# Performance work log

Hardware: AMD Instinct MI355X
Metric: run time of the kernel (lower is better)

## Reference

```python
import jax, jax.numpy as jnp
import numpy as np

S, B, T = 512, 256, 128


def setup_inputs() -> dict:
    key = jax.random.key(0)
    k1, k2, k3, k4, k5, k6 = jax.random.split(key, 6)
    emissions = jax.random.normal(k1, (S, B, T), dtype=jnp.float32)
    # realistic monotone mask: each sequence has a random length in [1, S]
    lengths = jax.random.randint(k2, (B,), 1, S + 1)
    mask = (jnp.arange(S)[:, None] < lengths[None, :]).astype(jnp.float32)  # [S,B]
    tags = jax.random.randint(k3, (S, B), 0, T)
    transitions = jax.random.normal(k4, (T, T), dtype=jnp.float32)
    start_transitions = jax.random.normal(k5, (T,), dtype=jnp.float32)
    stop_transitions = jax.random.normal(k6, (T,), dtype=jnp.float32)
    return {
        "emissions": emissions,
        "mask": mask,
        "tags": tags,
        "transitions": transitions,
        "start_transitions": start_transitions,
        "stop_transitions": stop_transitions,
    }


def reference(emissions, mask, tags, transitions, start_transitions, stop_transitions):
    seq_len, batch, num_tags = emissions.shape

    # ---- log-partition (forward algorithm) + viterbi score, fused scan ----
    init = start_transitions + emissions[0]  # [B,T]

    def part_step(carry, xs):
        fv, vv = carry  # forward var, viterbi var: [B,T]
        em, m = xs      # em: [B,T], m: [B]
        # scores[b, j, k] = em[b, j] + transitions[j, k]  (j=next tag, k=prev tag)
        scores = em[:, :, None] + transitions[None, :, :]          # [B,T,T]
        lse = jax.nn.logsumexp(fv[:, None, :] + scores, axis=2)     # [B,T]
        vmax = jnp.max(vv[:, None, :] + scores, axis=2)             # [B,T]
        fv = m[:, None] * lse + (1.0 - m)[:, None] * fv
        vv = m[:, None] * vmax + (1.0 - m)[:, None] * vv
        return (fv, vv), None

    (fv, vv), _ = jax.lax.scan(part_step, (init, init), (emissions[1:], mask[1:]))
    total_score = jax.nn.logsumexp(fv + stop_transitions, axis=1)   # [B]
    best_path_score = jnp.max(vv + stop_transitions, axis=1)        # [B]

    # ---- gold path score ----
    barange = jnp.arange(batch)
    tag0 = tags[0]
    rps0 = start_transitions[tag0] + emissions[0, barange, tag0] * mask[0]

    def rp_step(carry, xs):
        rps, prev = carry
        cur, em, m = xs  # cur:[B] int, em:[B,T], m:[B]
        rps = rps + transitions[prev, cur] * m
        rps = rps + jnp.take_along_axis(em, cur[:, None], axis=1)[:, 0] * m
        prev = jnp.where(m == 1.0, cur, prev)
        return (rps, prev), None

    (rps, prev), _ = jax.lax.scan(rp_step, (rps0, tag0), (tags[1:], emissions[1:], mask[1:]))
    real_path_score = rps + stop_transitions[prev]

    loss = jnp.mean(total_score - real_path_score)
    return loss, real_path_score, total_score, best_path_score
```

## Files before the change

### kernel.cpp

```cpp
#include <hip/hip_runtime.h>
#include <math.h>

#define S_LEN 512
#define BATCH 256
#define NTAG  128
#define EMSTRIDE (BATCH * NTAG)

typedef float f32x4 __attribute__((ext_vector_type(4)));

__device__ __forceinline__ int swz(int k) { return k + ((k >> 5) << 3); }

#define DPP_XOR1(x) __int_as_float(__builtin_amdgcn_mov_dpp(__float_as_int(x), 0xB1, 0xF, 0xF, false))
#define DPP_XOR2(x) __int_as_float(__builtin_amdgcn_mov_dpp(__float_as_int(x), 0x4E, 0xF, 0xF, false))

#define BAR() do {                                       \
    asm volatile("s_waitcnt lgkmcnt(0)" ::: "memory");   \
    __builtin_amdgcn_s_barrier();                        \
    __builtin_amdgcn_sched_barrier(0);                   \
  } while (0)

__device__ __forceinline__ float max3f(float a, float b, float c) {
  return fmaxf(fmaxf(a, b), c);
}

__global__ __launch_bounds__(512, 1)
void crf_fat_kernel(const float* __restrict__ emis,
                    const float* __restrict__ mask,
                    const int* __restrict__ tags,
                    const float* __restrict__ trans,
                    const float* __restrict__ startt,
                    const float* __restrict__ stopt,
                    float* __restrict__ out)
{
  const int blk = blockIdx.x;
  const int tid = threadIdx.x;

  __shared__ __align__(16) float sbuf[2][160];
  __shared__ float red[16];

  if (blk >= 2 * BATCH) {
    const int b = blk - 2 * BATCH;
    const int s = tid;
    float m  = mask[(size_t)s * BATCH + b];
    int  cur = tags[(size_t)s * BATCH + b];
    float part, lenp = m;
    if (s == 0) {
      part = startt[cur] + emis[(size_t)b * NTAG + cur] * m;
    } else {
      int prev = tags[(size_t)(s - 1) * BATCH + b];
      part = m * (trans[(size_t)prev * NTAG + cur] +
                  emis[((size_t)s * BATCH + b) * NTAG + cur]);
    }
#pragma unroll
    for (int d = 1; d <= 32; d <<= 1) {
      part += __shfl_xor(part, d);
      lenp += __shfl_xor(lenp, d);
    }
    const int glane = tid & 63, gwid = tid >> 6;
    if (glane == 0) { red[gwid] = part; red[8 + gwid] = lenp; }
    __syncthreads();
    if (tid == 0) {
      float rps = 0.f, lf = 0.f;
#pragma unroll
      for (int w = 0; w < 8; ++w) { rps += red[w]; lf += red[8 + w]; }
      int len = (int)(lf + 0.5f);
      int pf  = tags[(size_t)(len - 1) * BATCH + b];
      out[1 + b] = rps + stopt[pf];
    }
    return;
  }

  const int b    = blk >> 1;
  const int role = blk & 1;
  const int h    = tid & 3;
  const int j    = tid >> 2;
  const int lane = tid & 63;
  const int wid  = tid >> 6;
  const int base = 10 * h;

  int len;
  {
    float mv = mask[(size_t)tid * BATCH + b];
#pragma unroll
    for (int d = 1; d <= 32; d <<= 1) mv += __shfl_xor(mv, d);
    if (lane == 0) red[wid] = mv;
    __syncthreads();
    float ls = 0.f;
#pragma unroll
    for (int w = 0; w < 8; ++w) ls += red[w];
    len = (int)(ls + 0.5f);
    len = __builtin_amdgcn_readfirstlane(len);
  }

  const float* eb = emis + (size_t)b * NTAG + j;

  if (role == 0) {
    f32x4 E[8];
    {
      const float* tr = trans + (size_t)j * NTAG + 32 * h;
#pragma unroll
      for (int c = 0; c < 8; ++c) {
        f32x4 t = *(const f32x4*)(tr + 4 * c);
        E[c][0] = __expf(t[0]); E[c][1] = __expf(t[1]);
        E[c][2] = __expf(t[2]); E[c][3] = __expf(t[3]);
      }
    }
    if (h == 0) sbuf[0][swz(j)] = __expf(startt[j] + eb[0]);

    float e0 = eb[(size_t)1 * EMSTRIDE];
    float e1 = eb[(size_t)2 * EMSTRIDE];
    float e2 = eb[(size_t)3 * EMSTRIDE];
    float e3 = eb[(size_t)4 * EMSTRIDE];

    int Ew = 0, fin = 0;
    __syncthreads();

#define FSTEP(U, EMV, RENORM)                                                \
  {                                                                          \
    if (g + (U) >= len) { fin = (U) & 1; goto epi_f; }                       \
    const f32x4* wr = (const f32x4*)sbuf[(U) & 1];                           \
    float s0 = 0.f, s1 = 0.f, s2 = 0.f, s3 = 0.f, rw = 0.f;                  \
    _Pragma("unroll")                                                        \
    for (int c = 0; c < 8; ++c) {                                            \
      f32x4 w = wr[base + c];                                                \
      s0 = __builtin_fmaf(E[c][0], w[0], s0);                                \
      s1 = __builtin_fmaf(E[c][1], w[1], s1);                                \
      s2 = __builtin_fmaf(E[c][2], w[2], s2);                                \
      s3 = __builtin_fmaf(E[c][3], w[3], s3);                                \
      if (RENORM) { rw = max3f(rw, w[0], w[1]); rw = max3f(rw, w[2], w[3]); }\
    }                                                                        \
    float ex  = __expf(EMV);                                                 \
    float sum = (s0 + s1) + (s2 + s3);                                       \
    sum += DPP_XOR1(sum); sum += DPP_XOR2(sum);                              \
    float uf;                                                                \
    if (RENORM) {                                                            \
      rw = fmaxf(rw, DPP_XOR1(rw)); rw = fmaxf(rw, DPP_XOR2(rw));            \
      int ew = (int)((__float_as_uint(rw) >> 23) & 0xFF) - 126;              \
      Ew += ew;                                                              \
      float sw = __uint_as_float((unsigned)(127 - ew) << 23);                \
      uf = ex * sum * sw;                                                    \
    } else {                                                                 \
      uf = ex * sum;                                                         \
    }                                                                        \
    if (h == 0) sbuf[((U) + 1) & 1][swz(j)] = uf;                            \
    BAR();                                                                   \
  }

    for (int g = 1; g < S_LEN; g += 4) {
      int c0 = g + 4, c1 = g + 5, c2 = g + 6, c3 = g + 7;
      c0 = c0 < S_LEN ? c0 : S_LEN - 1;
      c1 = c1 < S_LEN ? c1 : S_LEN - 1;
      c2 = c2 < S_LEN ? c2 : S_LEN - 1;
      c3 = c3 < S_LEN ? c3 : S_LEN - 1;
      float n0 = eb[(size_t)c0 * EMSTRIDE];
      float n1 = eb[(size_t)c1 * EMSTRIDE];
      float n2 = eb[(size_t)c2 * EMSTRIDE];
      float n3 = eb[(size_t)c3 * EMSTRIDE];

      FSTEP(0, e0, 0)
      FSTEP(1, e1, 0)
      FSTEP(2, e2, 0)
      FSTEP(3, e3, 1)

      e0 = n0; e1 = n1; e2 = n2; e3 = n3;
    }
    fin = 0;

epi_f:
    {
      float W  = sbuf[fin][swz(j)];
      float es = __expf(stopt[j]);
      int q2 = fin ^ 1;
      if (h == 0) sbuf[q2][swz(j)] = W * es;
      __syncthreads();
      if (tid < 64) {
        float sA = sbuf[q2][swz(tid)] + sbuf[q2][swz(tid + 64)];
#pragma unroll
        for (int d = 1; d <= 32; d <<= 1) sA += __shfl_xor(sA, d);
        if (tid == 0) {
          const double LN2 = 0.6931471805599453;
          out[1 + BATCH + b] = (float)((double)Ew * LN2 + (double)__logf(sA));
        }
      }
    }
  } else {
    f32x4 T[8];
    {
      const float* tr = trans + (size_t)j * NTAG + 32 * h;
#pragma unroll
      for (int c = 0; c < 8; ++c) T[c] = *(const f32x4*)(tr + 4 * c);
    }
    if (h == 0) sbuf[0][swz(j)] = startt[j] + eb[0];

    float e0 = eb[(size_t)1 * EMSTRIDE];
    float e1 = eb[(size_t)2 * EMSTRIDE];
    float e2 = eb[(size_t)3 * EMSTRIDE];
    float e3 = eb[(size_t)4 * EMSTRIDE];

    int fin = 0;
    __syncthreads();

#define VSTEP(U, EMV)                                                        \
  {                                                                          \
    if (g + (U) >= len) { fin = (U) & 1; goto epi_v; }                       \
    const f32x4* vr = (const f32x4*)sbuf[(U) & 1];                           \
    float vmA = -3.0e38f, vmB = -3.0e38f;                                    \
    _Pragma("unroll")                                                        \
    for (int c = 0; c < 8; ++c) {                                            \
      f32x4 v = vr[base + c];                                                \
      vmA = max3f(vmA, v[0] + T[c][0], v[1] + T[c][1]);                      \
      vmB = max3f(vmB, v[2] + T[c][2], v[3] + T[c][3]);                      \
    }                                                                        \
    float vm = fmaxf(vmA, vmB);                                              \
    vm = fmaxf(vm, DPP_XOR1(vm)); vm = fmaxf(vm, DPP_XOR2(vm));              \
    float uv = EMV + vm;                                                     \
    if (h == 0) sbuf[((U) + 1) & 1][swz(j)] = uv;                            \
    BAR();                                                                   \
  }

    for (int g = 1; g < S_LEN; g += 4) {
      int c0 = g + 4, c1 = g + 5, c2 = g + 6, c3 = g + 7;
      c0 = c0 < S_LEN ? c0 : S_LEN - 1;
      c1 = c1 < S_LEN ? c1 : S_LEN - 1;
      c2 = c2 < S_LEN ? c2 : S_LEN - 1;
      c3 = c3 < S_LEN ? c3 : S_LEN - 1;
      float n0 = eb[(size_t)c0 * EMSTRIDE];
      float n1 = eb[(size_t)c1 * EMSTRIDE];
      float n2 = eb[(size_t)c2 * EMSTRIDE];
      float n3 = eb[(size_t)c3 * EMSTRIDE];

      VSTEP(0, e0)
      VSTEP(1, e1)
      VSTEP(2, e2)
      VSTEP(3, e3)

      e0 = n0; e1 = n1; e2 = n2; e3 = n3;
    }
    fin = 0;

epi_v:
    {
      float V = sbuf[fin][swz(j)];
      float a = V + stopt[j];
      int q2 = fin ^ 1;
      if (h == 0) sbuf[q2][swz(j)] = a;
      __syncthreads();
      if (tid < 64) {
        float mB = fmaxf(sbuf[q2][swz(tid)], sbuf[q2][swz(tid + 64)]);
#pragma unroll
        for (int d = 1; d <= 32; d <<= 1) mB = fmaxf(mB, __shfl_xor(mB, d));
        if (tid == 0) out[1 + 2 * BATCH + b] = mB;
      }
    }
  }
}

__global__ __launch_bounds__(256, 1)
void crf_loss_kernel(float* __restrict__ out)
{
  const int tid = threadIdx.x;
  float dft = out[1 + BATCH + tid] - out[1 + tid];
#pragma unroll
  for (int d = 1; d <= 32; d <<= 1) dft += __shfl_xor(dft, d);
  __shared__ float rs[4];
  const int lane = tid & 63, wid = tid >> 6;
  if (lane == 0) rs[wid] = dft;
  __syncthreads();
  if (tid == 0)
    out[0] = ((rs[0] + rs[1]) + (rs[2] + rs[3])) * (1.0f / BATCH);
}

extern "C" void kernel_launch(void* const* d_in, const int* in_sizes, int n_in,
                              void* d_out, int out_size, void* d_ws, size_t ws_size,
                              hipStream_t stream)
{
  const float* emis   = (const float*)d_in[0];
  const float* mask   = (const float*)d_in[1];
  const int*   tags   = (const int*)d_in[2];
  const float* trans  = (const float*)d_in[3];
  const float* startt = (const float*)d_in[4];
  const float* stopt  = (const float*)d_in[5];
  float* out = (float*)d_out;

  crf_fat_kernel<<<3 * BATCH, 512, 0, stream>>>(emis, mask, tags, trans,
                                                startt, stopt, out);
  crf_loss_kernel<<<1, 256, 0, stream>>>(out);
}
```

Baseline: 209.2 us.

## Split CRF recursions into forward and backward halves meeting at the midpoint

Splits each sequence's forward-algorithm and Viterbi recursions into a forward half and a backward half that run in separate blocks. The halves meet at the midpoint and are combined by a new kernel: a dot product for the log-partition and a max of sums for Viterbi. This roughly halves the serial chain of barrier-separated steps per block. It also shrinks blocks to 256 threads with 2 lanes per tag and packed 2-wide math, and adds workspace traffic plus an extra kernel launch.

```diff
diff --git a/kernel.cpp b/kernel.cpp
--- a/kernel.cpp
+++ b/kernel.cpp
@@ -7,11 +7,16 @@
 #define EMSTRIDE (BATCH * NTAG)
 
 typedef float f32x4 __attribute__((ext_vector_type(4)));
-
-__device__ __forceinline__ int swz(int k) { return k + ((k >> 5) << 3); }
+typedef float f32x2 __attribute__((ext_vector_type(2)));
+
+__device__ __forceinline__ int lidx(int k) { return k + ((k >> 6) << 2); }
+__device__ __forceinline__ f32x2 lo2(f32x4 v){ f32x2 r; r[0]=v[0]; r[1]=v[1]; return r; }
+__device__ __forceinline__ f32x2 hi2(f32x4 v){ f32x2 r; r[0]=v[2]; r[1]=v[3]; return r; }
+__device__ __forceinline__ f32x2 pmax2(f32x2 a, f32x2 b){
+  f32x2 r; r[0]=fmaxf(a[0],b[0]); r[1]=fmaxf(a[1],b[1]); return r;
+}
 
 #define DPP_XOR1(x) __int_as_float(__builtin_amdgcn_mov_dpp(__float_as_int(x), 0xB1, 0xF, 0xF, false))
-#define DPP_XOR2(x) __int_as_float(__builtin_amdgcn_mov_dpp(__float_as_int(x), 0x4E, 0xF, 0xF, false))
 
 #define BAR() do {                                       \
     asm volatile("s_waitcnt lgkmcnt(0)" ::: "memory");   \
@@ -19,50 +24,53 @@
     __builtin_amdgcn_sched_barrier(0);                   \
   } while (0)
 
-__device__ __forceinline__ float max3f(float a, float b, float c) {
-  return fmaxf(fmaxf(a, b), c);
-}
-
-__global__ __launch_bounds__(512, 1)
+__global__ __launch_bounds__(256, 1)
 void crf_fat_kernel(const float* __restrict__ emis,
                     const float* __restrict__ mask,
                     const int* __restrict__ tags,
                     const float* __restrict__ trans,
                     const float* __restrict__ startt,
                     const float* __restrict__ stopt,
+                    float* __restrict__ ws,
+                    int* __restrict__ ewbuf,
                     float* __restrict__ out)
 {
-  const int blk = blockIdx.x;
-  const int tid = threadIdx.x;
-
-  __shared__ __align__(16) float sbuf[2][160];
-  __shared__ float red[16];
-
-  if (blk >= 2 * BATCH) {
-    const int b = blk - 2 * BATCH;
-    const int s = tid;
-    float m  = mask[(size_t)s * BATCH + b];
-    int  cur = tags[(size_t)s * BATCH + b];
-    float part, lenp = m;
-    if (s == 0) {
-      part = startt[cur] + emis[(size_t)b * NTAG + cur] * m;
-    } else {
-      int prev = tags[(size_t)(s - 1) * BATCH + b];
-      part = m * (trans[(size_t)prev * NTAG + cur] +
-                  emis[((size_t)s * BATCH + b) * NTAG + cur]);
+  const int blk  = blockIdx.x;
+  const int tid  = threadIdx.x;
+  const int role = blk >> 8;
+  const int b    = blk & 255;
+  const int lane = tid & 63;
+  const int wid  = tid >> 6;
+
+  __shared__ __align__(16) float sbuf[2][144];
+  __shared__ float red[8];
+
+  if (role == 4) {
+    float part = 0.f, lenp = 0.f;
+#pragma unroll
+    for (int rep = 0; rep < 2; ++rep) {
+      int s = tid + rep * 256;
+      float m  = mask[(size_t)s * BATCH + b];
+      int  cur = tags[(size_t)s * BATCH + b];
+      if (s == 0) {
+        part += startt[cur] + emis[(size_t)b * NTAG + cur] * m;
+      } else {
+        int prev = tags[(size_t)(s - 1) * BATCH + b];
+        part += m * (trans[(size_t)prev * NTAG + cur] +
+                     emis[((size_t)s * BATCH + b) * NTAG + cur]);
+      }
+      lenp += m;
     }
 #pragma unroll
     for (int d = 1; d <= 32; d <<= 1) {
       part += __shfl_xor(part, d);
       lenp += __shfl_xor(lenp, d);
     }
-    const int glane = tid & 63, gwid = tid >> 6;
-    if (glane == 0) { red[gwid] = part; red[8 + gwid] = lenp; }
+    if (lane == 0) { red[wid] = part; red[4 + wid] = lenp; }
     __syncthreads();
     if (tid == 0) {
-      float rps = 0.f, lf = 0.f;
-#pragma unroll
-      for (int w = 0; w < 8; ++w) { rps += red[w]; lf += red[8 + w]; }
+      float rps = (red[0] + red[1]) + (red[2] + red[3]);
+      float lf  = (red[4] + red[5]) + (red[6] + red[7]);
       int len = (int)(lf + 0.5f);
       int pf  = tags[(size_t)(len - 1) * BATCH + b];
       out[1 + b] = rps + stopt[pf];
@@ -70,188 +78,332 @@
     return;
   }
 
-  const int b    = blk >> 1;
-  const int role = blk & 1;
-  const int h    = tid & 3;
-  const int j    = tid >> 2;
-  const int lane = tid & 63;
-  const int wid  = tid >> 6;
-  const int base = 10 * h;
+  const int p    = tid >> 1;
+  const int h    = tid & 1;
+  const int widx = lidx(p);
 
   int len;
   {
-    float mv = mask[(size_t)tid * BATCH + b];
+    float mv = mask[(size_t)tid * BATCH + b] +
+               mask[(size_t)(tid + 256) * BATCH + b];
 #pragma unroll
     for (int d = 1; d <= 32; d <<= 1) mv += __shfl_xor(mv, d);
     if (lane == 0) red[wid] = mv;
     __syncthreads();
-    float ls = 0.f;
-#pragma unroll
-    for (int w = 0; w < 8; ++w) ls += red[w];
+    float ls = (red[0] + red[1]) + (red[2] + red[3]);
     len = (int)(ls + 0.5f);
     len = __builtin_amdgcn_readfirstlane(len);
   }
-
-  const float* eb = emis + (size_t)b * NTAG + j;
+  const int sm     = (len - 1) >> 1;
+  const int nsteps = len - 1 - sm;
+  const float* eb  = emis + (size_t)b * NTAG + p;
 
   if (role == 0) {
-    f32x4 E[8];
-    {
-      const float* tr = trans + (size_t)j * NTAG + 32 * h;
-#pragma unroll
-      for (int c = 0; c < 8; ++c) {
+    f32x2 E2[32];
+    {
+      const float* tr = trans + (size_t)p * NTAG + 64 * h;
+#pragma unroll
+      for (int c = 0; c < 16; ++c) {
         f32x4 t = *(const f32x4*)(tr + 4 * c);
-        E[c][0] = __expf(t[0]); E[c][1] = __expf(t[1]);
-        E[c][2] = __expf(t[2]); E[c][3] = __expf(t[3]);
+        f32x2 a, bb;
+        a[0] = __expf(t[0]); a[1] = __expf(t[1]);
+        bb[0] = __expf(t[2]); bb[1] = __expf(t[3]);
+        E2[2*c] = a; E2[2*c+1] = bb;
       }
     }
-    if (h == 0) sbuf[0][swz(j)] = __expf(startt[j] + eb[0]);
-
+    if (h == 0) sbuf[0][widx] = __expf(startt[p] + eb[0]);
     float e0 = eb[(size_t)1 * EMSTRIDE];
     float e1 = eb[(size_t)2 * EMSTRIDE];
     float e2 = eb[(size_t)3 * EMSTRIDE];
     float e3 = eb[(size_t)4 * EMSTRIDE];
-
     int Ew = 0, fin = 0;
     __syncthreads();
 
-#define FSTEP(U, EMV, RENORM)                                                \
-  {                                                                          \
-    if (g + (U) >= len) { fin = (U) & 1; goto epi_f; }                       \
-    const f32x4* wr = (const f32x4*)sbuf[(U) & 1];                           \
-    float s0 = 0.f, s1 = 0.f, s2 = 0.f, s3 = 0.f, rw = 0.f;                  \
-    _Pragma("unroll")                                                        \
-    for (int c = 0; c < 8; ++c) {                                            \
-      f32x4 w = wr[base + c];                                                \
-      s0 = __builtin_fmaf(E[c][0], w[0], s0);                                \
-      s1 = __builtin_fmaf(E[c][1], w[1], s1);                                \
-      s2 = __builtin_fmaf(E[c][2], w[2], s2);                                \
-      s3 = __builtin_fmaf(E[c][3], w[3], s3);                                \
-      if (RENORM) { rw = max3f(rw, w[0], w[1]); rw = max3f(rw, w[2], w[3]); }\
-    }                                                                        \
-    float ex  = __expf(EMV);                                                 \
-    float sum = (s0 + s1) + (s2 + s3);                                       \
-    sum += DPP_XOR1(sum); sum += DPP_XOR2(sum);                              \
-    float uf;                                                                \
-    if (RENORM) {                                                            \
-      rw = fmaxf(rw, DPP_XOR1(rw)); rw = fmaxf(rw, DPP_XOR2(rw));            \
-      int ew = (int)((__float_as_uint(rw) >> 23) & 0xFF) - 126;              \
-      Ew += ew;                                                              \
-      float sw = __uint_as_float((unsigned)(127 - ew) << 23);                \
-      uf = ex * sum * sw;                                                    \
-    } else {                                                                 \
-      uf = ex * sum;                                                         \
-    }                                                                        \
-    if (h == 0) sbuf[((U) + 1) & 1][swz(j)] = uf;                            \
-    BAR();                                                                   \
+#define FSTEP(U, EXV, RENORM)                                                 \
+  {                                                                           \
+    if (g + (U) > sm) { fin = (U) & 1; goto epi_f; }                          \
+    const f32x4* wr = (const f32x4*)(sbuf[(U) & 1] + 68 * h);                 \
+    f32x2 a0 = {0.f, 0.f}, a1 = {0.f, 0.f}, r2 = {0.f, 0.f};                  \
+    _Pragma("unroll")                                                         \
+    for (int c = 0; c < 16; ++c) {                                            \
+      f32x4 w = wr[c];                                                        \
+      f32x2 wl = lo2(w), wh = hi2(w);                                         \
+      a0 = a0 + E2[2*c] * wl;                                                 \
+      a1 = a1 + E2[2*c+1] * wh;                                               \
+      if (RENORM) r2 = pmax2(r2, pmax2(wl, wh));                              \
+    }                                                                         \
+    f32x2 as = a0 + a1;                                                       \
+    float sum = as[0] + as[1];                                                \
+    sum += DPP_XOR1(sum);                                                     \
+    float uf;                                                                 \
+    if (RENORM) {                                                             \
+      float rw = fmaxf(r2[0], r2[1]);                                         \
+      rw = fmaxf(rw, DPP_XOR1(rw));                                           \
+      int ew = (int)((__float_as_uint(rw) >> 23) & 0xFF) - 126;               \
+      Ew += ew;                                                               \
+      float swc = __uint_as_float((unsigned)(127 - ew) << 23);                \
+      uf = (EXV) * sum * swc;                                                 \
+    } else {                                                                  \
+      uf = (EXV) * sum;                                                       \
+    }                                                                         \
+    if (h == 0) sbuf[((U) + 1) & 1][widx] = uf;                               \
+    BAR();                                                                    \
   }
 
     for (int g = 1; g < S_LEN; g += 4) {
-      int c0 = g + 4, c1 = g + 5, c2 = g + 6, c3 = g + 7;
-      c0 = c0 < S_LEN ? c0 : S_LEN - 1;
-      c1 = c1 < S_LEN ? c1 : S_LEN - 1;
-      c2 = c2 < S_LEN ? c2 : S_LEN - 1;
-      c3 = c3 < S_LEN ? c3 : S_LEN - 1;
+      int c0 = g + 4 < S_LEN ? g + 4 : S_LEN - 1;
+      int c1 = g + 5 < S_LEN ? g + 5 : S_LEN - 1;
+      int c2 = g + 6 < S_LEN ? g + 6 : S_LEN - 1;
+      int c3 = g + 7 < S_LEN ? g + 7 : S_LEN - 1;
       float n0 = eb[(size_t)c0 * EMSTRIDE];
       float n1 = eb[(size_t)c1 * EMSTRIDE];
       float n2 = eb[(size_t)c2 * EMSTRIDE];
       float n3 = eb[(size_t)c3 * EMSTRIDE];
-
-      FSTEP(0, e0, 0)
-      FSTEP(1, e1, 0)
-      FSTEP(2, e2, 0)
-      FSTEP(3, e3, 1)
-
+      float x0 = __expf(e0), x1 = __expf(e1);
+      float x2 = __expf(e2), x3 = __expf(e3);
+      FSTEP(0, x0, 0)
+      FSTEP(1, x1, 0)
+      FSTEP(2, x2, 0)
+      FSTEP(3, x3, 1)
       e0 = n0; e1 = n1; e2 = n2; e3 = n3;
     }
     fin = 0;
-
 epi_f:
     {
-      float W  = sbuf[fin][swz(j)];
-      float es = __expf(stopt[j]);
-      int q2 = fin ^ 1;
-      if (h == 0) sbuf[q2][swz(j)] = W * es;
-      __syncthreads();
-      if (tid < 64) {
-        float sA = sbuf[q2][swz(tid)] + sbuf[q2][swz(tid + 64)];
-#pragma unroll
-        for (int d = 1; d <= 32; d <<= 1) sA += __shfl_xor(sA, d);
-        if (tid == 0) {
-          const double LN2 = 0.6931471805599453;
-          out[1 + BATCH + b] = (float)((double)Ew * LN2 + (double)__logf(sA));
-        }
+      if (tid < 128) ws[(size_t)b * 512 + tid] = sbuf[fin][lidx(tid)];
+      if (tid == 0) ewbuf[b] = Ew;
+    }
+  } else if (role == 1) {
+    f32x2 E2[32];
+    {
+      const float* tc = trans + p + (size_t)(64 * h) * NTAG;
+#pragma unroll
+      for (int e = 0; e < 32; ++e) {
+        f32x2 a;
+        a[0] = __expf(tc[(size_t)(2*e)     * NTAG]);
+        a[1] = __expf(tc[(size_t)(2*e + 1) * NTAG]);
+        E2[e] = a;
       }
     }
-  } else {
-    f32x4 T[8];
-    {
-      const float* tr = trans + (size_t)j * NTAG + 32 * h;
-#pragma unroll
-      for (int c = 0; c < 8; ++c) T[c] = *(const f32x4*)(tr + 4 * c);
-    }
-    if (h == 0) sbuf[0][swz(j)] = startt[j] + eb[0];
-
+    if (h == 0) {
+      float st = stopt[p];
+      float y = (nsteps > 0) ? __expf(st + eb[(size_t)(len - 1) * EMSTRIDE])
+                             : __expf(st);
+      sbuf[0][widx] = y;
+    }
+    int s0i = len - 2;     s0i = s0i < 0 ? 0 : s0i;
+    int s1i = len - 3;     s1i = s1i < 0 ? 0 : s1i;
+    int s2i = len - 4;     s2i = s2i < 0 ? 0 : s2i;
+    int s3i = len - 5;     s3i = s3i < 0 ? 0 : s3i;
+    float e0 = eb[(size_t)s0i * EMSTRIDE];
+    float e1 = eb[(size_t)s1i * EMSTRIDE];
+    float e2 = eb[(size_t)s2i * EMSTRIDE];
+    float e3 = eb[(size_t)s3i * EMSTRIDE];
+    int Ew = 0, fin = 0;
+    __syncthreads();
+
+#define BSTEP(U, EXV, RENORM)                                                 \
+  {                                                                           \
+    if (gi + (U) >= nsteps) { fin = (U) & 1; goto epi_b; }                    \
+    const f32x4* wr = (const f32x4*)(sbuf[(U) & 1] + 68 * h);                 \
+    f32x2 a0 = {0.f, 0.f}, a1 = {0.f, 0.f}, r2 = {0.f, 0.f};                  \
+    _Pragma("unroll")                                                         \
+    for (int c = 0; c < 16; ++c) {                                            \
+      f32x4 w = wr[c];                                                        \
+      f32x2 wl = lo2(w), wh = hi2(w);                                         \
+      a0 = a0 + E2[2*c] * wl;                                                 \
+      a1 = a1 + E2[2*c+1] * wh;                                               \
+      if (RENORM) r2 = pmax2(r2, pmax2(wl, wh));                              \
+    }                                                                         \
+    f32x2 as = a0 + a1;                                                       \
+    float sum = as[0] + as[1];                                                \
+    sum += DPP_XOR1(sum);                                                     \
+    float exm = (gi + (U) == nsteps - 1) ? 1.0f : (EXV);                      \
+    float uf;                                                                 \
+    if (RENORM) {                                                             \
+      float rw = fmaxf(r2[0], r2[1]);                                         \
+      rw = fmaxf(rw, DPP_XOR1(rw));                                           \
+      int ew = (int)((__float_as_uint(rw) >> 23) & 0xFF) - 126;               \
+      Ew += ew;                                                               \
+      float swc = __uint_as_float((unsigned)(127 - ew) << 23);                \
+      uf = exm * sum * swc;                                                   \
+    } else {                                                                  \
+      uf = exm * sum;                                                         \
+    }                                                                         \
+    if (h == 0) sbuf[((U) + 1) & 1][widx] = uf;                               \
+    BAR();                                                                    \
+  }
+
+    for (int gi = 0; gi < S_LEN; gi += 4) {
+      int c0 = len - 2 - (gi + 4); c0 = c0 < 0 ? 0 : c0;
+      int c1 = len - 2 - (gi + 5); c1 = c1 < 0 ? 0 : c1;
+      int c2 = len - 2 - (gi + 6); c2 = c2 < 0 ? 0 : c2;
+      int c3 = len - 2 - (gi + 7); c3 = c3 < 0 ? 0 : c3;
+      float n0 = eb[(size_t)c0 * EMSTRIDE];
+      float n1 = eb[(size_t)c1 * EMSTRIDE];
+      float n2 = eb[(size_t)c2 * EMSTRIDE];
+      float n3 = eb[(size_t)c3 * EMSTRIDE];
+      float x0 = __expf(e0), x1 = __expf(e1);
+      float x2 = __expf(e2), x3 = __expf(e3);
+      BSTEP(0, x0, 0)
+      BSTEP(1, x1, 0)
+      BSTEP(2, x2, 0)
+      BSTEP(3, x3, 1)
+      e0 = n0; e1 = n1; e2 = n2; e3 = n3;
+    }
+    fin = 0;
+epi_b:
+    {
+      if (tid < 128) ws[(size_t)b * 512 + 128 + tid] = sbuf[fin][lidx(tid)];
+      if (tid == 0) ewbuf[BATCH + b] = Ew;
+    }
+  } else if (role == 2) {
+    f32x2 T2[32];
+    {
+      const float* tr = trans + (size_t)p * NTAG + 64 * h;
+#pragma unroll
+      for (int c = 0; c < 16; ++c) {
+        f32x4 t = *(const f32x4*)(tr + 4 * c);
+        T2[2*c]   = lo2(t);
+        T2[2*c+1] = hi2(t);
+      }
+    }
+    if (h == 0) sbuf[0][widx] = startt[p] + eb[0];
     float e0 = eb[(size_t)1 * EMSTRIDE];
     float e1 = eb[(size_t)2 * EMSTRIDE];
     float e2 = eb[(size_t)3 * EMSTRIDE];
     float e3 = eb[(size_t)4 * EMSTRIDE];
-
     int fin = 0;
     __syncthreads();
 
-#define VSTEP(U, EMV)                                                        \
-  {                                                                          \
-    if (g + (U) >= len) { fin = (U) & 1; goto epi_v; }                       \
-    const f32x4* vr = (const f32x4*)sbuf[(U) & 1];                           \
-    float vmA = -3.0e38f, vmB = -3.0e38f;                                    \
-    _Pragma("unroll")                                                        \
-    for (int c = 0; c < 8; ++c) {                                            \
-      f32x4 v = vr[base + c];                                                \
-      vmA = max3f(vmA, v[0] + T[c][0], v[1] + T[c][1]);                      \
-      vmB = max3f(vmB, v[2] + T[c][2], v[3] + T[c][3]);                      \
-    }                                                                        \
-    float vm = fmaxf(vmA, vmB);                                              \
-    vm = fmaxf(vm, DPP_XOR1(vm)); vm = fmaxf(vm, DPP_XOR2(vm));              \
-    float uv = EMV + vm;                                                     \
-    if (h == 0) sbuf[((U) + 1) & 1][swz(j)] = uv;                            \
-    BAR();                                                                   \
+#define VSTEP(U, EMV)                                                         \
+  {                                                                           \
+    if (g + (U) > sm) { fin = (U) & 1; goto epi_v; }                          \
+    const f32x4* vr = (const f32x4*)(sbuf[(U) & 1] + 68 * h);                 \
+    f32x2 m2 = {-3.0e38f, -3.0e38f};                                          \
+    _Pragma("unroll")                                                         \
+    for (int c = 0; c < 16; ++c) {                                            \
+      f32x4 v = vr[c];                                                        \
+      m2 = pmax2(m2, pmax2(lo2(v) + T2[2*c], hi2(v) + T2[2*c+1]));            \
+    }                                                                         \
+    float vm = fmaxf(m2[0], m2[1]);                                           \
+    vm = fmaxf(vm, DPP_XOR1(vm));                                             \
+    float uv = (EMV) + vm;                                                    \
+    if (h == 0) sbuf[((U) + 1) & 1][widx] = uv;                               \
+    BAR();                                                                    \
   }
 
     for (int g = 1; g < S_LEN; g += 4) {
-      int c0 = g + 4, c1 = g + 5, c2 = g + 6, c3 = g + 7;
-      c0 = c0 < S_LEN ? c0 : S_LEN - 1;
-      c1 = c1 < S_LEN ? c1 : S_LEN - 1;
-      c2 = c2 < S_LEN ? c2 : S_LEN - 1;
-      c3 = c3 < S_LEN ? c3 : S_LEN - 1;
+      int c0 = g + 4 < S_LEN ? g + 4 : S_LEN - 1;
+      int c1 = g + 5 < S_LEN ? g + 5 : S_LEN - 1;
+      int c2 = g + 6 < S_LEN ? g + 6 : S_LEN - 1;
+      int c3 = g + 7 < S_LEN ? g + 7 : S_LEN - 1;
       float n0 = eb[(size_t)c0 * EMSTRIDE];
       float n1 = eb[(size_t)c1 * EMSTRIDE];
       float n2 = eb[(size_t)c2 * EMSTRIDE];
       float n3 = eb[(size_t)c3 * EMSTRIDE];
-
       VSTEP(0, e0)
       VSTEP(1, e1)
       VSTEP(2, e2)
       VSTEP(3, e3)
-
       e0 = n0; e1 = n1; e2 = n2; e3 = n3;
     }
     fin = 0;
-
 epi_v:
     {
-      float V = sbuf[fin][swz(j)];
-      float a = V + stopt[j];
-      int q2 = fin ^ 1;
-      if (h == 0) sbuf[q2][swz(j)] = a;
-      __syncthreads();
-      if (tid < 64) {
-        float mB = fmaxf(sbuf[q2][swz(tid)], sbuf[q2][swz(tid + 64)]);
-#pragma unroll
-        for (int d = 1; d <= 32; d <<= 1) mB = fmaxf(mB, __shfl_xor(mB, d));
-        if (tid == 0) out[1 + 2 * BATCH + b] = mB;
+      if (tid < 128) ws[(size_t)b * 512 + 256 + tid] = sbuf[fin][lidx(tid)];
+    }
+  } else {
+    f32x2 T2[32];
+    {
+      const float* tc = trans + p + (size_t)(64 * h) * NTAG;
+#pragma unroll
+      for (int e = 0; e < 32; ++e) {
+        f32x2 a;
+        a[0] = tc[(size_t)(2*e)     * NTAG];
+        a[1] = tc[(size_t)(2*e + 1) * NTAG];
+        T2[e] = a;
       }
     }
+    if (h == 0) {
+      float st = stopt[p];
+      float y = (nsteps > 0) ? st + eb[(size_t)(len - 1) * EMSTRIDE] : st;
+      sbuf[0][widx] = y;
+    }
+    int s0i = len - 2;     s0i = s0i < 0 ? 0 : s0i;
+    int s1i = len - 3;     s1i = s1i < 0 ? 0 : s1i;
+    int s2i = len - 4;     s2i = s2i < 0 ? 0 : s2i;
+    int s3i = len - 5;     s3i = s3i < 0 ? 0 : s3i;
+    float e0 = eb[(size_t)s0i * EMSTRIDE];
+    float e1 = eb[(size_t)s1i * EMSTRIDE];
+    float e2 = eb[(size_t)s2i * EMSTRIDE];
+    float e3 = eb[(size_t)s3i * EMSTRIDE];
+    int fin = 0;
+    __syncthreads();
+
+#define WSTEP(U, EMV)                                                         \
+  {                                                                           \
+    if (gi + (U) >= nsteps) { fin = (U) & 1; goto epi_w; }                    \
+    const f32x4* vr = (const f32x4*)(sbuf[(U) & 1] + 68 * h);                 \
+    f32x2 m2 = {-3.0e38f, -3.0e38f};                                          \
+    _Pragma("unroll")                                                         \
+    for (int c = 0; c < 16; ++c) {                                            \
+      f32x4 v = vr[c];                                                        \
+      m2 = pmax2(m2, pmax2(lo2(v) + T2[2*c], hi2(v) + T2[2*c+1]));            \
+    }                                                                         \
+    float vm = fmaxf(m2[0], m2[1]);                                           \
+    vm = fmaxf(vm, DPP_XOR1(vm));                                             \
+    float uv = (gi + (U) == nsteps - 1) ? vm : vm + (EMV);                    \
+    if (h == 0) sbuf[((U) + 1) & 1][widx] = uv;                               \
+    BAR();                                                                    \
+  }
+
+    for (int gi = 0; gi < S_LEN; gi += 4) {
+      int c0 = len - 2 - (gi + 4); c0 = c0 < 0 ? 0 : c0;
+      int c1 = len - 2 - (gi + 5); c1 = c1 < 0 ? 0 : c1;
+      int c2 = len - 2 - (gi + 6); c2 = c2 < 0 ? 0 : c2;
+      int c3 = len - 2 - (gi + 7); c3 = c3 < 0 ? 0 : c3;
+      float n0 = eb[(size_t)c0 * EMSTRIDE];
+      float n1 = eb[(size_t)c1 * EMSTRIDE];
+      float n2 = eb[(size_t)c2 * EMSTRIDE];
+      float n3 = eb[(size_t)c3 * EMSTRIDE];
+      WSTEP(0, e0)
+      WSTEP(1, e1)
+      WSTEP(2, e2)
+      WSTEP(3, e3)
+      e0 = n0; e1 = n1; e2 = n2; e3 = n3;
+    }
+    fin = 0;
+epi_w:
+    {
+      if (tid < 128) ws[(size_t)b * 512 + 384 + tid] = sbuf[fin][lidx(tid)];
+    }
+  }
+}
+
+__global__ __launch_bounds__(128, 1)
+void crf_combine_kernel(const float* __restrict__ ws,
+                        const int* __restrict__ ewbuf,
+                        float* __restrict__ out)
+{
+  const int b = blockIdx.x, k = threadIdx.x;
+  const float* base = ws + (size_t)b * 512;
+  float t1 = base[k] * base[128 + k];
+  float m1 = base[256 + k] + base[384 + k];
+#pragma unroll
+  for (int d = 1; d <= 32; d <<= 1) {
+    t1 += __shfl_xor(t1, d);
+    m1 = fmaxf(m1, __shfl_xor(m1, d));
+  }
+  __shared__ float rs[2], rm[2];
+  const int lane = k & 63, wid = k >> 6;
+  if (lane == 0) { rs[wid] = t1; rm[wid] = m1; }
+  __syncthreads();
+  if (k == 0) {
+    const double LN2 = 0.6931471805599453;
+    int Et = ewbuf[b] + ewbuf[BATCH + b];
+    out[1 + BATCH + b]     = (float)((double)Et * LN2 + (double)__logf(rs[0] + rs[1]));
+    out[1 + 2 * BATCH + b] = fmaxf(rm[0], rm[1]);
   }
 }
 
@@ -282,7 +434,11 @@
   const float* stopt  = (const float*)d_in[5];
   float* out = (float*)d_out;
 
-  crf_fat_kernel<<<3 * BATCH, 512, 0, stream>>>(emis, mask, tags, trans,
-                                                startt, stopt, out);
+  float* wsf   = (float*)d_ws;
+  int*   ewbuf = (int*)(wsf + 512 * BATCH);
+
+  crf_fat_kernel<<<5 * BATCH, 256, 0, stream>>>(emis, mask, tags, trans,
+                                                startt, stopt, wsf, ewbuf, out);
+  crf_combine_kernel<<<BATCH, 128, 0, stream>>>(wsf, ewbuf, out);
   crf_loss_kernel<<<1, 256, 0, stream>>>(out);
 }
```

Result: no change. 210.0 us (+0.4%).
